# Kernel tuning notes

Hardware: AMD Instinct MI355X
Metric: run time of the kernel (lower is better)

## Reference

```python
import jax, jax.numpy as jnp
import numpy as np

IMG, P, S, E, B = 224, 16, 8, 128, 64
N = (IMG - P) // S + 1          # patches per spatial dim (27)
L = N * N                       # num patches (729)
K = P * P                       # patch area (256)


def _flat_patch_idx():
    # flattened pixel index for each (patch, within-patch) element, shape [L, K]
    base = jnp.arange(N) * S            # top-left corner of each patch row/col
    off = jnp.arange(P)
    rows = base[:, None] + off[None, :]  # [N, P]
    hh = rows[:, None, :, None]          # [N,1,P,1]
    ww = rows[None, :, None, :]          # [1,N,1,P]
    return (hh * IMG + ww).reshape(L, K)  # row-major over patch positions, i*P+j within patch (matches torch Unfold)


def setup_inputs() -> dict:
    key = jax.random.key(0)
    k = jax.random.split(key, 5)
    x = jax.random.normal(k[0], (B, 3, IMG, IMG), dtype=jnp.float32)
    W_enc = jax.random.normal(k[1], (3, E, K), dtype=jnp.float32) * 0.02
    b_enc = jax.random.normal(k[2], (3, E), dtype=jnp.float32) * 0.02
    W_dec = jax.random.normal(k[3], (3, K, E), dtype=jnp.float32) * 0.02
    b_dec = jax.random.normal(k[4], (3, K), dtype=jnp.float32) * 0.02
    return {"x": x, "W_enc": W_enc, "b_enc": b_enc, "W_dec": W_dec, "b_dec": b_dec}


def reference(x, W_enc, b_enc, W_dec, b_dec):
    flat = _flat_patch_idx()                         # [L, K] int indices, static
    Bn = x.shape[0]
    # unfold: gather overlapping patches -> [B, 3, L, K]
    patches = x.reshape(Bn, 3, IMG * IMG)[:, :, flat]
    # per-channel linear encode: [B,3,L,E]
    emb = jnp.einsum('bclk,cek->bcle', patches, W_enc) + b_enc[:, None, :]
    # per-channel linear decode: [B,3,L,K]
    rec = jnp.einsum('bcle,cke->bclk', emb, W_dec) + b_dec[:, None, :]
    # fold: overlap-add scatter back to image
    fi = flat.reshape(-1)
    out = jnp.zeros((Bn, 3, IMG * IMG), x.dtype).at[:, :, fi].add(rec.reshape(Bn, 3, L * K))
    # normalization = fold(unfold(ones)) = per-pixel overlap count
    count = jnp.zeros((IMG * IMG,), x.dtype).at[fi].add(jnp.ones((L * K,), x.dtype))
    return (out / count).reshape(Bn, 3, IMG, IMG)
```

## Files before the change

kernel.cpp:

```cpp
#include <hip/hip_runtime.h>

#define IMG   224
#define IMG2  (IMG*IMG)
#define NN    27
#define KK    256
#define EE    128
#define NSTRIP 28
#define SCOLS 232
#define RSTR  136

typedef float f32x4 __attribute__((ext_vector_type(4)));
typedef short s16x8 __attribute__((ext_vector_type(8)));

__device__ __forceinline__ unsigned short f2bf(float f) {
    unsigned int u = __float_as_uint(f);
    u = (u + 0x7fffu + ((u >> 16) & 1u)) >> 16;
    return (unsigned short)u;
}
__device__ __forceinline__ float bf2f(unsigned short u) {
    return __uint_as_float((unsigned int)u << 16);
}
__device__ __forceinline__ uint2 pack4(f32x4 r) {
    uint2 u;
    asm("v_cvt_pk_bf16_f32 %0, %1, %2" : "=v"(u.x) : "v"(r.x), "v"(r.y));
    asm("v_cvt_pk_bf16_f32 %0, %1, %2" : "=v"(u.y) : "v"(r.z), "v"(r.w));
    return u;
}

__global__ void pack_M(const float* __restrict__ W_enc, const float* __restrict__ W_dec,
                       const float* __restrict__ b_enc, const float* __restrict__ b_dec,
                       unsigned short* __restrict__ APK, float* __restrict__ v) {
    int k = blockIdx.x, c = blockIdx.y, j = threadIdx.x;
    const float* wd = W_dec + ((size_t)c*KK + k)*EE;
    const float* we = W_enc + (size_t)c*EE*KK + j;
    float acc = 0.f;
    #pragma unroll 8
    for (int e = 0; e < EE; ++e) acc = fmaf(wd[e], we[(size_t)e*KK], acc);
    int kf = k >> 4, kr = k & 15, jb = j >> 5, g = (j >> 3) & 3, i = j & 7;
    APK[(size_t)c*65536 + (((kf*8 + jb)*64) + g*16 + kr)*8 + i] = f2bf(acc);

    __shared__ float pv[128];
    if (j < EE) pv[j] = wd[j] * b_enc[c*EE + j];
    __syncthreads();
    for (int off = 64; off > 0; off >>= 1) {
        if (j < off) pv[j] += pv[j + off];
        __syncthreads();
    }
    if (j == 0) v[c*KK + k] = pv[0] + b_dec[c*KK + k];
}

__global__ __launch_bounds__(256, 4)
void patch_ae_mfma(const float* __restrict__ x, const unsigned short* __restrict__ APK,
                   const float* __restrict__ v, float* __restrict__ out) {
    const int hid = blockIdx.x + NSTRIP*(blockIdx.y + 3*blockIdx.z);
    const int lid = (hid & 7)*672 + (hid >> 3);
    const int s  = lid % NSTRIP;
    const int t2 = lid / NSTRIP;
    const int c  = t2 % 3;
    const int b  = t2 / 3;

    const int tid  = threadIdx.x;
    const int lane = tid & 63, wave = tid >> 6;

    __shared__ __align__(16) unsigned short strip[24*SCOLS];
    __shared__ __align__(16) unsigned short rec[2][30][RSTR];
    __shared__ __align__(16) float vsh[256];

    vsh[tid] = v[c*256 + tid];
    if (tid < RSTR) {
        rec[0][0][tid] = 0; rec[0][28][tid] = 0;
        rec[1][0][tid] = 0; rec[1][28][tid] = 0;
    }

    const int prow    = wave >> 1;
    const int kq      = wave & 1;
    const int rowbase = prow ? 0 : 8;
    const int kfbase  = prow*8 + kq*4;
    const int g = lane >> 4, lr = lane & 15;
    const int jx0 = (g & 1)*8;
    const int c1 = (lr <= 10) ? (128 + 8*lr) : 208;

    const int kfu = __builtin_amdgcn_readfirstlane(kfbase);
    const char* sbase = (const char*)(APK + (size_t)c*65536) + (size_t)kfu*8192;
    const int voff0 = lane*16;
    const int voff1 = voff0 + 8192;
    const int voff2 = voff0 + 16384;
    const int voff3 = voff0 + 24576;

#define AISSUE(DST, VOFF, OFFSTR)                                   \
    asm volatile("global_load_dwordx4 %0, %1, %2 offset:" OFFSTR    \
                 : "=v"(DST) : "v"(VOFF), "s"(sbase));

    s16x8 aA0, aA1, aA2, aA3, aB0, aB1, aB2, aB3;
    AISSUE(aA0, voff0, "0")    AISSUE(aA1, voff1, "0")
    AISSUE(aA2, voff2, "0")    AISSUE(aA3, voff3, "0")
    AISSUE(aB0, voff0, "1024") AISSUE(aB1, voff1, "1024")
    AISSUE(aB2, voff2, "1024") AISSUE(aB3, voff3, "1024")

    {
        const float* xb = x + (size_t)(b*3 + c)*IMG2;
        const int ybase = 8*s - 8;
        #pragma unroll
        for (int it = 0; it < 3; ++it) {
            int ci = tid + it*256;
            if (ci < 672) {
                int r  = ci / 28;
                int cc = ci - r*28;
                int yr = ybase + r;
                float4 lo = make_float4(0.f,0.f,0.f,0.f), hi = lo;
                if ((unsigned)yr < IMG) {
                    const float4* src = (const float4*)(xb + (size_t)yr*IMG + cc*8);
                    lo = src[0]; hi = src[1];
                }
                uint2 u0 = pack4((f32x4){lo.x, lo.y, lo.z, lo.w});
                uint2 u1 = pack4((f32x4){hi.x, hi.y, hi.z, hi.w});
                *((uint4*)&strip[r*SCOLS + cc*8]) = make_uint4(u0.x, u0.y, u1.x, u1.y);
            }
        }
    }
    __syncthreads();

    {
        f32x4 acc[4][2];
        #pragma unroll
        for (int f = 0; f < 4; ++f)
            #pragma unroll
            for (int pf = 0; pf < 2; ++pf)
                acc[f][pf] = (f32x4){0.f, 0.f, 0.f, 0.f};

#define MFMA2(AF, B0, B1, F)                                                         \
        acc[F][0] = __builtin_amdgcn_mfma_f32_16x16x32_bf16(AF, B0, acc[F][0], 0, 0, 0); \
        acc[F][1] = __builtin_amdgcn_mfma_f32_16x16x32_bf16(AF, B1, acc[F][1], 0, 0, 0);

#define MSTEP(JB, A0, A1, A2, A3, WAITSTR)                                           \
        {                                                                            \
            const int jy = 2*(JB) + (g >> 1);                                        \
            const unsigned short* srow = &strip[(rowbase + jy)*SCOLS + jx0];         \
            s16x8 bf0 = *((const s16x8*)&srow[8*lr]);                                \
            s16x8 bf1 = *((const s16x8*)&srow[c1]);                                  \
            asm volatile("s_waitcnt vmcnt(" WAITSTR ")");                            \
            __builtin_amdgcn_sched_barrier(0);                                       \
            __builtin_amdgcn_s_setprio(1);                                           \
            MFMA2(A0, bf0, bf1, 0) MFMA2(A1, bf0, bf1, 1)                            \
            MFMA2(A2, bf0, bf1, 2) MFMA2(A3, bf0, bf1, 3)                            \
            __builtin_amdgcn_s_setprio(0);                                           \
        }

        MSTEP(0, aA0, aA1, aA2, aA3, "4")
        AISSUE(aA0, voff0, "2048")        AISSUE(aA1, voff1, "2048")
        AISSUE(aA2, voff2, "2048")        AISSUE(aA3, voff3, "2048")
        MSTEP(1, aB0, aB1, aB2, aB3, "4")
        AISSUE(aB0, voff0, "3072")        AISSUE(aB1, voff1, "3072")
        AISSUE(aB2, voff2, "3072")        AISSUE(aB3, voff3, "3072")
        MSTEP(2, aA0, aA1, aA2, aA3, "4")
        AISSUE(aA0, voff0 + 4096, "0")    AISSUE(aA1, voff1 + 4096, "0")
        AISSUE(aA2, voff2 + 4096, "0")    AISSUE(aA3, voff3 + 4096, "0")
        MSTEP(3, aB0, aB1, aB2, aB3, "4")
        AISSUE(aB0, voff0 + 4096, "1024") AISSUE(aB1, voff1 + 4096, "1024")
        AISSUE(aB2, voff2 + 4096, "1024") AISSUE(aB3, voff3 + 4096, "1024")
        MSTEP(4, aA0, aA1, aA2, aA3, "4")
        AISSUE(aA0, voff0 + 4096, "2048") AISSUE(aA1, voff1 + 4096, "2048")
        AISSUE(aA2, voff2 + 4096, "2048") AISSUE(aA3, voff3 + 4096, "2048")
        MSTEP(5, aB0, aB1, aB2, aB3, "4")
        AISSUE(aB0, voff0 + 4096, "3072") AISSUE(aB1, voff1 + 4096, "3072")
        AISSUE(aB2, voff2 + 4096, "3072") AISSUE(aB3, voff3 + 4096, "3072")
        MSTEP(6, aA0, aA1, aA2, aA3, "4")
        MSTEP(7, aB0, aB1, aB2, aB3, "0")
#undef MSTEP
#undef MFMA2
#undef AISSUE

        #pragma unroll
        for (int f = 0; f < 4; ++f) {
            int klocal = kq*64 + f*16 + g*4;
            f32x4 bias = *((const f32x4*)&vsh[prow*128 + klocal]);
            #pragma unroll
            for (int pf = 0; pf < 2; ++pf) {
                f32x4 r = acc[f][pf] + bias;
                int pidx = pf*16 + lr + 1;
                if (pidx >= 28) pidx = 29;
                *((uint2*)&rec[prow][pidx][klocal]) = pack4(r);
            }
        }
    }
    __syncthreads();

    if (tid < 224) {
        const int q  = tid % 28;
        const int ry = tid / 28;
        const int v1 = (q < 27);
        const int v0 = (q > 0);
        const int h0 = (s < NSTRIP-1);
        const int h1 = (s > 0);
        const int shift = (v0 & v1) + (h0 & h1);
        const float inv = __int_as_float(0x3f800000 - (shift << 23));
        const int ro = ry*16;

        float sum[8];
        #pragma unroll
        for (int d = 0; d < 8; ++d) sum[d] = 0.f;
        if (h0) {
            s16x8 rr = *((const s16x8*)&rec[0][q+1][ro]);
            s16x8 ll = *((const s16x8*)&rec[0][q][ro + 8]);
            #pragma unroll
            for (int d = 0; d < 8; ++d)
                sum[d] += bf2f((unsigned short)rr[d]) + bf2f((unsigned short)ll[d]);
        }
        if (h1) {
            s16x8 rr = *((const s16x8*)&rec[1][q+1][ro]);
            s16x8 ll = *((const s16x8*)&rec[1][q][ro + 8]);
            #pragma unroll
            for (int d = 0; d < 8; ++d)
                sum[d] += bf2f((unsigned short)rr[d]) + bf2f((unsigned short)ll[d]);
        }
        float* orow = out + (size_t)(b*3 + c)*IMG2 + (size_t)(8*s + ry)*IMG + 8*q;
        f32x4 o0 = {sum[0]*inv, sum[1]*inv, sum[2]*inv, sum[3]*inv};
        f32x4 o1 = {sum[4]*inv, sum[5]*inv, sum[6]*inv, sum[7]*inv};
        *((f32x4*)orow)       = o0;
        *((f32x4*)(orow + 4)) = o1;
    }
}

extern "C" void kernel_launch(void* const* d_in, const int* in_sizes, int n_in,
                              void* d_out, int out_size, void* d_ws, size_t ws_size,
                              hipStream_t stream) {
    (void)in_sizes; (void)n_in; (void)out_size; (void)ws_size;
    const float* x     = (const float*)d_in[0];
    const float* W_enc = (const float*)d_in[1];
    const float* b_enc = (const float*)d_in[2];
    const float* W_dec = (const float*)d_in[3];
    const float* b_dec = (const float*)d_in[4];
    float* out = (float*)d_out;

    float*          v   = (float*)d_ws;
    unsigned short* APK = (unsigned short*)((char*)d_ws + 4096);

    pack_M<<<dim3(KK, 3), 256, 0, stream>>>(W_enc, W_dec, b_enc, b_dec, APK, v);
    patch_ae_mfma<<<dim3(NSTRIP, 3, 64), 256, 0, stream>>>(x, APK, v, out);
}
```

Before: 47.89 us.

## Make blocks persistent over seven strips with register-resident weights and ring buffer

Each block now processes seven consecutive row strips instead of one. The full per-wave A-matrix fragment (32 registers of bf16x8) is loaded once and kept in registers, and only the next 8 image rows are streamed into a 32-row shared ring buffer, with the prefetch overlapped with the MFMAs. This removes the repeated weight loads and the overlapping strip reloads paid per block, but it cuts the grid to 768 blocks and lowers occupancy through launch bounds of 2 and heavy register use. It also serialises the strips within a block behind extra barriers.

```diff
diff --git a/kernel.cpp b/kernel.cpp
--- a/kernel.cpp
+++ b/kernel.cpp
@@ -5,7 +5,6 @@
 #define NN    27
 #define KK    256
 #define EE    128
-#define NSTRIP 28
 #define SCOLS 232
 #define RSTR  136
 
@@ -49,20 +48,21 @@
     if (j == 0) v[c*KK + k] = pv[0] + b_dec[c*KK + k];
 }
 
-__global__ __launch_bounds__(256, 4)
-void patch_ae_mfma(const float* __restrict__ x, const unsigned short* __restrict__ APK,
+__global__ __launch_bounds__(256, 2)
+void patch_ae_loop(const float* __restrict__ x, const unsigned short* __restrict__ APK,
                    const float* __restrict__ v, float* __restrict__ out) {
-    const int hid = blockIdx.x + NSTRIP*(blockIdx.y + 3*blockIdx.z);
-    const int lid = (hid & 7)*672 + (hid >> 3);
-    const int s  = lid % NSTRIP;
-    const int t2 = lid / NSTRIP;
-    const int c  = t2 % 3;
-    const int b  = t2 / 3;
+    const int hid = blockIdx.x;
+    const int lid = (hid & 7)*96 + (hid >> 3);
+    const int q   = lid & 3;
+    const int t2  = lid >> 2;
+    const int c   = t2 % 3;
+    const int b   = t2 / 3;
+    const int s0  = 7*q;
 
     const int tid  = threadIdx.x;
     const int lane = tid & 63, wave = tid >> 6;
 
-    __shared__ __align__(16) unsigned short strip[24*SCOLS];
+    __shared__ __align__(16) unsigned short ring[32*SCOLS];
     __shared__ __align__(16) unsigned short rec[2][30][RSTR];
     __shared__ __align__(16) float vsh[256];
 
@@ -72,103 +72,107 @@
         rec[1][0][tid] = 0; rec[1][28][tid] = 0;
     }
 
-    const int prow    = wave >> 1;
-    const int kq      = wave & 1;
-    const int rowbase = prow ? 0 : 8;
-    const int kfbase  = prow*8 + kq*4;
+    const int prow   = wave >> 1;
+    const int kq     = wave & 1;
+    const int kfbase = prow*8 + kq*4;
     const int g = lane >> 4, lr = lane & 15;
     const int jx0 = (g & 1)*8;
     const int c1 = (lr <= 10) ? (128 + 8*lr) : 208;
+    const int rowoff = prow ? -8 : 0;
 
     const int kfu = __builtin_amdgcn_readfirstlane(kfbase);
-    const char* sbase = (const char*)(APK + (size_t)c*65536) + (size_t)kfu*8192;
-    const int voff0 = lane*16;
-    const int voff1 = voff0 + 8192;
-    const int voff2 = voff0 + 16384;
-    const int voff3 = voff0 + 24576;
-
-#define AISSUE(DST, VOFF, OFFSTR)                                   \
+    const char* abase = (const char*)(APK + (size_t)c*65536) + (size_t)kfu*8192;
+    const int vf0 = lane*16,        vf0b = vf0 + 4096;
+    const int vf1 = vf0 + 8192,     vf1b = vf1 + 4096;
+    const int vf2 = vf0 + 16384,    vf2b = vf2 + 4096;
+    const int vf3 = vf0 + 24576,    vf3b = vf3 + 4096;
+
+#define ALD(VAR, VOFF, OFFSTR)                                      \
     asm volatile("global_load_dwordx4 %0, %1, %2 offset:" OFFSTR    \
-                 : "=v"(DST) : "v"(VOFF), "s"(sbase));
-
-    s16x8 aA0, aA1, aA2, aA3, aB0, aB1, aB2, aB3;
-    AISSUE(aA0, voff0, "0")    AISSUE(aA1, voff1, "0")
-    AISSUE(aA2, voff2, "0")    AISSUE(aA3, voff3, "0")
-    AISSUE(aB0, voff0, "1024") AISSUE(aB1, voff1, "1024")
-    AISSUE(aB2, voff2, "1024") AISSUE(aB3, voff3, "1024")
-
-    {
-        const float* xb = x + (size_t)(b*3 + c)*IMG2;
-        const int ybase = 8*s - 8;
-        #pragma unroll
-        for (int it = 0; it < 3; ++it) {
-            int ci = tid + it*256;
-            if (ci < 672) {
-                int r  = ci / 28;
-                int cc = ci - r*28;
-                int yr = ybase + r;
-                float4 lo = make_float4(0.f,0.f,0.f,0.f), hi = lo;
-                if ((unsigned)yr < IMG) {
-                    const float4* src = (const float4*)(xb + (size_t)yr*IMG + cc*8);
-                    lo = src[0]; hi = src[1];
-                }
-                uint2 u0 = pack4((f32x4){lo.x, lo.y, lo.z, lo.w});
-                uint2 u1 = pack4((f32x4){hi.x, hi.y, hi.z, hi.w});
-                *((uint4*)&strip[r*SCOLS + cc*8]) = make_uint4(u0.x, u0.y, u1.x, u1.y);
-            }
+                 : "=v"(VAR) : "v"(VOFF), "s"(abase));
+
+    s16x8 a0_0,a0_1,a0_2,a0_3,a0_4,a0_5,a0_6,a0_7;
+    s16x8 a1_0,a1_1,a1_2,a1_3,a1_4,a1_5,a1_6,a1_7;
+    s16x8 a2_0,a2_1,a2_2,a2_3,a2_4,a2_5,a2_6,a2_7;
+    s16x8 a3_0,a3_1,a3_2,a3_3,a3_4,a3_5,a3_6,a3_7;
+    ALD(a0_0, vf0,  "0")    ALD(a0_1, vf0,  "1024") ALD(a0_2, vf0,  "2048") ALD(a0_3, vf0,  "3072")
+    ALD(a0_4, vf0b, "0")    ALD(a0_5, vf0b, "1024") ALD(a0_6, vf0b, "2048") ALD(a0_7, vf0b, "3072")
+    ALD(a1_0, vf1,  "0")    ALD(a1_1, vf1,  "1024") ALD(a1_2, vf1,  "2048") ALD(a1_3, vf1,  "3072")
+    ALD(a1_4, vf1b, "0")    ALD(a1_5, vf1b, "1024") ALD(a1_6, vf1b, "2048") ALD(a1_7, vf1b, "3072")
+    ALD(a2_0, vf2,  "0")    ALD(a2_1, vf2,  "1024") ALD(a2_2, vf2,  "2048") ALD(a2_3, vf2,  "3072")
+    ALD(a2_4, vf2b, "0")    ALD(a2_5, vf2b, "1024") ALD(a2_6, vf2b, "2048") ALD(a2_7, vf2b, "3072")
+    ALD(a3_0, vf3,  "0")    ALD(a3_1, vf3,  "1024") ALD(a3_2, vf3,  "2048") ALD(a3_3, vf3,  "3072")
+    ALD(a3_4, vf3b, "0")    ALD(a3_5, vf3b, "1024") ALD(a3_6, vf3b, "2048") ALD(a3_7, vf3b, "3072")
+#undef ALD
+
+    const float* xb = x + (size_t)(b*3 + c)*IMG2;
+
+    #pragma unroll
+    for (int it = 0; it < 3; ++it) {
+        int ci = tid + it*256;
+        if (ci < 672) {
+            int r  = ci / 28, cc = ci - (ci/28)*28;
+            int ar = 8*s0 - 8 + r;
+            int yr = ar < 0 ? 0 : (ar > 223 ? 223 : ar);
+            const float4* src = (const float4*)(xb + (size_t)yr*IMG + cc*8);
+            float4 lo = src[0], hi = src[1];
+            uint2 u0 = pack4((f32x4){lo.x, lo.y, lo.z, lo.w});
+            uint2 u1 = pack4((f32x4){hi.x, hi.y, hi.z, hi.w});
+            *((uint4*)&ring[(ar & 31)*SCOLS + cc*8]) = make_uint4(u0.x, u0.y, u1.x, u1.y);
         }
     }
     __syncthreads();
-
-    {
+    asm volatile("s_waitcnt vmcnt(0)");
+    __builtin_amdgcn_sched_barrier(0);
+
+    const int rr  = tid / 28;
+    const int cc2 = tid - 28*(tid/28);
+
+    const int eq  = tid % 28, ery = tid / 28;
+    const int ev1 = (eq < 27), ev0 = (eq > 0);
+    const int ero = ery*16;
+
+#define MFMA2(AF, B0, B1, F)                                                             \
+        acc[F][0] = __builtin_amdgcn_mfma_f32_16x16x32_bf16(AF, B0, acc[F][0], 0, 0, 0); \
+        acc[F][1] = __builtin_amdgcn_mfma_f32_16x16x32_bf16(AF, B1, acc[F][1], 0, 0, 0);
+
+#define MSTEP(JB, A0, A1, A2, A3)                                                    \
+        {                                                                            \
+            const int jy = 2*(JB) + (g >> 1);                                        \
+            const unsigned short* srow = &ring[((rowb + jy) & 31)*SCOLS + jx0];      \
+            s16x8 bf0 = *((const s16x8*)&srow[8*lr]);                                \
+            s16x8 bf1 = *((const s16x8*)&srow[c1]);                                  \
+            __builtin_amdgcn_s_setprio(1);                                           \
+            MFMA2(A0, bf0, bf1, 0) MFMA2(A1, bf0, bf1, 1)                            \
+            MFMA2(A2, bf0, bf1, 2) MFMA2(A3, bf0, bf1, 3)                            \
+            __builtin_amdgcn_s_setprio(0);                                           \
+        }
+
+    #pragma unroll 1
+    for (int s = s0; s < s0 + 7; ++s) {
+        f32x4 ga0, ga1;
+        if (tid < 224) {
+            int yr = 8*(s+2) + rr; if (yr > 223) yr = 223;
+            int voffx = yr*(IMG*4) + cc2*32;
+            asm volatile("global_load_dwordx4 %0, %1, %2"           : "=v"(ga0) : "v"(voffx), "s"(xb));
+            asm volatile("global_load_dwordx4 %0, %1, %2 offset:16" : "=v"(ga1) : "v"(voffx), "s"(xb));
+        }
+
         f32x4 acc[4][2];
         #pragma unroll
         for (int f = 0; f < 4; ++f)
             #pragma unroll
             for (int pf = 0; pf < 2; ++pf)
                 acc[f][pf] = (f32x4){0.f, 0.f, 0.f, 0.f};
-
-#define MFMA2(AF, B0, B1, F)                                                         \
-        acc[F][0] = __builtin_amdgcn_mfma_f32_16x16x32_bf16(AF, B0, acc[F][0], 0, 0, 0); \
-        acc[F][1] = __builtin_amdgcn_mfma_f32_16x16x32_bf16(AF, B1, acc[F][1], 0, 0, 0);
-
-#define MSTEP(JB, A0, A1, A2, A3, WAITSTR)                                           \
-        {                                                                            \
-            const int jy = 2*(JB) + (g >> 1);                                        \
-            const unsigned short* srow = &strip[(rowbase + jy)*SCOLS + jx0];         \
-            s16x8 bf0 = *((const s16x8*)&srow[8*lr]);                                \
-            s16x8 bf1 = *((const s16x8*)&srow[c1]);                                  \
-            asm volatile("s_waitcnt vmcnt(" WAITSTR ")");                            \
-            __builtin_amdgcn_sched_barrier(0);                                       \
-            __builtin_amdgcn_s_setprio(1);                                           \
-            MFMA2(A0, bf0, bf1, 0) MFMA2(A1, bf0, bf1, 1)                            \
-            MFMA2(A2, bf0, bf1, 2) MFMA2(A3, bf0, bf1, 3)                            \
-            __builtin_amdgcn_s_setprio(0);                                           \
-        }
-
-        MSTEP(0, aA0, aA1, aA2, aA3, "4")
-        AISSUE(aA0, voff0, "2048")        AISSUE(aA1, voff1, "2048")
-        AISSUE(aA2, voff2, "2048")        AISSUE(aA3, voff3, "2048")
-        MSTEP(1, aB0, aB1, aB2, aB3, "4")
-        AISSUE(aB0, voff0, "3072")        AISSUE(aB1, voff1, "3072")
-        AISSUE(aB2, voff2, "3072")        AISSUE(aB3, voff3, "3072")
-        MSTEP(2, aA0, aA1, aA2, aA3, "4")
-        AISSUE(aA0, voff0 + 4096, "0")    AISSUE(aA1, voff1 + 4096, "0")
-        AISSUE(aA2, voff2 + 4096, "0")    AISSUE(aA3, voff3 + 4096, "0")
-        MSTEP(3, aB0, aB1, aB2, aB3, "4")
-        AISSUE(aB0, voff0 + 4096, "1024") AISSUE(aB1, voff1 + 4096, "1024")
-        AISSUE(aB2, voff2 + 4096, "1024") AISSUE(aB3, voff3 + 4096, "1024")
-        MSTEP(4, aA0, aA1, aA2, aA3, "4")
-        AISSUE(aA0, voff0 + 4096, "2048") AISSUE(aA1, voff1 + 4096, "2048")
-        AISSUE(aA2, voff2 + 4096, "2048") AISSUE(aA3, voff3 + 4096, "2048")
-        MSTEP(5, aB0, aB1, aB2, aB3, "4")
-        AISSUE(aB0, voff0 + 4096, "3072") AISSUE(aB1, voff1 + 4096, "3072")
-        AISSUE(aB2, voff2 + 4096, "3072") AISSUE(aB3, voff3 + 4096, "3072")
-        MSTEP(6, aA0, aA1, aA2, aA3, "4")
-        MSTEP(7, aB0, aB1, aB2, aB3, "0")
-#undef MSTEP
-#undef MFMA2
-#undef AISSUE
+        const int rowb = 8*s + rowoff;
+        MSTEP(0, a0_0, a1_0, a2_0, a3_0)
+        MSTEP(1, a0_1, a1_1, a2_1, a3_1)
+        MSTEP(2, a0_2, a1_2, a2_2, a3_2)
+        MSTEP(3, a0_3, a1_3, a2_3, a3_3)
+        MSTEP(4, a0_4, a1_4, a2_4, a3_4)
+        MSTEP(5, a0_5, a1_5, a2_5, a3_5)
+        MSTEP(6, a0_6, a1_6, a2_6, a3_6)
+        MSTEP(7, a0_7, a1_7, a2_7, a3_7)
 
         #pragma unroll
         for (int f = 0; f < 4; ++f) {
@@ -182,43 +186,49 @@
                 *((uint2*)&rec[prow][pidx][klocal]) = pack4(r);
             }
         }
-    }
-    __syncthreads();
-
-    if (tid < 224) {
-        const int q  = tid % 28;
-        const int ry = tid / 28;
-        const int v1 = (q < 27);
-        const int v0 = (q > 0);
-        const int h0 = (s < NSTRIP-1);
-        const int h1 = (s > 0);
-        const int shift = (v0 & v1) + (h0 & h1);
-        const float inv = __int_as_float(0x3f800000 - (shift << 23));
-        const int ro = ry*16;
-
-        float sum[8];
-        #pragma unroll
-        for (int d = 0; d < 8; ++d) sum[d] = 0.f;
-        if (h0) {
-            s16x8 rr = *((const s16x8*)&rec[0][q+1][ro]);
-            s16x8 ll = *((const s16x8*)&rec[0][q][ro + 8]);
+        __syncthreads();
+
+        if (tid < 224) {
+            asm volatile("s_waitcnt vmcnt(0)");
+            __builtin_amdgcn_sched_barrier(0);
+            uint2 u0 = pack4(ga0);
+            uint2 u1 = pack4(ga1);
+            int ar2 = 8*(s+2) + rr;
+            *((uint4*)&ring[(ar2 & 31)*SCOLS + cc2*8]) = make_uint4(u0.x, u0.y, u1.x, u1.y);
+        }
+
+        if (tid < 224) {
+            const int h0 = (s < 27);
+            const int h1 = (s > 0);
+            const int shift = (ev0 & ev1) + (h0 & h1);
+            const float inv = __int_as_float(0x3f800000 - (shift << 23));
+            float sum[8];
             #pragma unroll
-            for (int d = 0; d < 8; ++d)
-                sum[d] += bf2f((unsigned short)rr[d]) + bf2f((unsigned short)ll[d]);
-        }
-        if (h1) {
-            s16x8 rr = *((const s16x8*)&rec[1][q+1][ro]);
-            s16x8 ll = *((const s16x8*)&rec[1][q][ro + 8]);
-            #pragma unroll
-            for (int d = 0; d < 8; ++d)
-                sum[d] += bf2f((unsigned short)rr[d]) + bf2f((unsigned short)ll[d]);
-        }
-        float* orow = out + (size_t)(b*3 + c)*IMG2 + (size_t)(8*s + ry)*IMG + 8*q;
-        f32x4 o0 = {sum[0]*inv, sum[1]*inv, sum[2]*inv, sum[3]*inv};
-        f32x4 o1 = {sum[4]*inv, sum[5]*inv, sum[6]*inv, sum[7]*inv};
-        *((f32x4*)orow)       = o0;
-        *((f32x4*)(orow + 4)) = o1;
-    }
+            for (int d = 0; d < 8; ++d) sum[d] = 0.f;
+            if (h0) {
+                s16x8 rrv = *((const s16x8*)&rec[0][eq+1][ero]);
+                s16x8 llv = *((const s16x8*)&rec[0][eq][ero + 8]);
+                #pragma unroll
+                for (int d = 0; d < 8; ++d)
+                    sum[d] += bf2f((unsigned short)rrv[d]) + bf2f((unsigned short)llv[d]);
+            }
+            if (h1) {
+                s16x8 rrv = *((const s16x8*)&rec[1][eq+1][ero]);
+                s16x8 llv = *((const s16x8*)&rec[1][eq][ero + 8]);
+                #pragma unroll
+                for (int d = 0; d < 8; ++d)
+                    sum[d] += bf2f((unsigned short)rrv[d]) + bf2f((unsigned short)llv[d]);
+            }
+            float* orow = out + (size_t)(b*3 + c)*IMG2 + (size_t)(8*s + ery)*IMG + 8*eq;
+            f32x4 o0 = {sum[0]*inv, sum[1]*inv, sum[2]*inv, sum[3]*inv};
+            f32x4 o1 = {sum[4]*inv, sum[5]*inv, sum[6]*inv, sum[7]*inv};
+            *((f32x4*)orow)       = o0;
+            *((f32x4*)(orow + 4)) = o1;
+        }
+        __syncthreads();
+    }
+#undef MSTEP
+#undef MFMA2
 }
 
 extern "C" void kernel_launch(void* const* d_in, const int* in_sizes, int n_in,
@@ -236,5 +246,5 @@
     unsigned short* APK = (unsigned short*)((char*)d_ws + 4096);
 
     pack_M<<<dim3(KK, 3), 256, 0, stream>>>(W_enc, W_dec, b_enc, b_dec, APK, v);
-    patch_ae_mfma<<<dim3(NSTRIP, 3, 64), 256, 0, stream>>>(x, APK, v, out);
-}
+    patch_ae_loop<<<dim3(768), 256, 0, stream>>>(x, APK, v, out);
+}
```

Result: faster. 42.36 us (-11.6%).
